# Performance work log

Measured on AMD Instinct MI355X. Metric: run time of the kernel, lower is better.

The kernel has to match this reference:

```python
import jax, jax.numpy as jnp
import numpy as np

NUM_EXPERTS = 8
IN_FEATURES = 2048
OUT_FEATURES = 2048
TOTAL_TOKENS = 32768


def setup_inputs() -> dict:
    key = jax.random.key(0)
    k1, k2, k3 = jax.random.split(key, 3)
    input_tokens = jax.random.normal(k1, (TOTAL_TOKENS, IN_FEATURES), dtype=jnp.float32)
    expert_assignments = jax.random.randint(k2, (TOTAL_TOKENS,), 0, NUM_EXPERTS, dtype=jnp.int32)
    # kaiming_uniform_ with a=sqrt(2): bound = sqrt(6 / ((1 + a^2) * fan_in)) = sqrt(2 / fan_in)
    bound = float(np.sqrt(2.0 / IN_FEATURES))
    weight = jax.random.uniform(k3, (NUM_EXPERTS, OUT_FEATURES, IN_FEATURES),
                                dtype=jnp.float32, minval=-bound, maxval=bound)
    return {"input_tokens": input_tokens, "expert_assignments": expert_assignments, "weight": weight}


def reference(input_tokens, expert_assignments, weight):
    # Grouped GEMM: out[t] = input_tokens[t] @ weight[assign[t]].T
    # Each token belongs to exactly one expert, so masked accumulation over the
    # small fixed expert set reproduces the original sort+per-expert-mm+scatter math.
    num_experts = weight.shape[0]
    out = jnp.zeros((input_tokens.shape[0], weight.shape[1]), dtype=input_tokens.dtype)
    for e in range(num_experts):
        mask = (expert_assignments == e)[:, None]  # [T, 1]
        # zero out tokens not owned by this expert before the GEMM so the
        # contribution is exact (matmul of zero rows yields zero rows)
        xe = jnp.where(mask, input_tokens, 0.0)  # [T, in]
        out = out + xe @ weight[e].T  # [T, out]
    return out
```

## Files before the change

### kernel.cpp

```cpp
#include <hip/hip_runtime.h>
#include <hip/hip_bf16.h>

#define NEXP 8
#define KIN 2048
#define NOUT 2048
#define NTOK 32768

#define BM 128
#define BN 128
#define BK 32

#define NBLK (NTOK / 256)
#define MAXTILE (NTOK / BM + NEXP - 1)

typedef unsigned int u32;
typedef unsigned short u16;
typedef __bf16 bf16x8 __attribute__((ext_vector_type(8)));
typedef float f32x4 __attribute__((ext_vector_type(4)));

__device__ __forceinline__ u16 f2bf(float f) {
    u32 u = __float_as_uint(f);
    u += 0x7FFFu + ((u >> 16) & 1u);
    return (u16)(u >> 16);
}

__device__ __forceinline__ void load_lds16(const void* g, void* l) {
    __builtin_amdgcn_global_load_lds(
        (const __attribute__((address_space(1))) u32*)g,
        (__attribute__((address_space(3))) u32*)l, 16, 0, 0);
}

__global__ void rank_k(const int* __restrict__ assign, int* __restrict__ counts,
                       int* __restrict__ rank, int* __restrict__ blockBase) {
    __shared__ int lc[NEXP];
    int t = blockIdx.x * 256 + threadIdx.x;
    if (threadIdx.x < NEXP) lc[threadIdx.x] = 0;
    __syncthreads();
    int e = assign[t];
    rank[t] = atomicAdd(&lc[e], 1);
    __syncthreads();
    if (threadIdx.x < NEXP)
        blockBase[blockIdx.x * NEXP + threadIdx.x] =
            atomicAdd(&counts[threadIdx.x], lc[threadIdx.x]);
}

__global__ void prefix_k(int* __restrict__ ctrl, int4* __restrict__ tileTable) {
    if (threadIdx.x == 0) {
        int ts = 0, tile = 0;
        for (int e = 0; e < NEXP; e++) {
            ctrl[8 + e] = ts;
            int c = ctrl[e];
            int ntile = (c + BM - 1) / BM;
            for (int i = 0; i < ntile; i++)
                tileTable[tile++] = make_int4(ts + i * BM, ts + c, e, 0);
            ts += c;
        }
        ctrl[8 + NEXP] = ts;
        for (; tile < MAXTILE; tile++) tileTable[tile] = make_int4(0, 0, 0, 0);
    }
}

__global__ void scatter_k(const int* __restrict__ assign, const int* __restrict__ ctrl,
                          const int* __restrict__ rank, const int* __restrict__ blockBase,
                          int* __restrict__ list) {
    __shared__ int base[NEXP];
    int t = blockIdx.x * 256 + threadIdx.x;
    if (threadIdx.x < NEXP)
        base[threadIdx.x] = ctrl[8 + threadIdx.x] +
                            blockBase[blockIdx.x * NEXP + threadIdx.x];
    __syncthreads();
    list[base[assign[t]] + rank[t]] = t;
}

__global__ void conv_k(const float* __restrict__ src, u16* __restrict__ dst) {
    size_t i = ((size_t)blockIdx.x * 256 + threadIdx.x) << 3;
    const float4* s = (const float4*)(src + i);
    float4 f0 = s[0], f1 = s[1];
    uint4 o;
    o.x = (u32)f2bf(f0.x) | ((u32)f2bf(f0.y) << 16);
    o.y = (u32)f2bf(f0.z) | ((u32)f2bf(f0.w) << 16);
    o.z = (u32)f2bf(f1.x) | ((u32)f2bf(f1.y) << 16);
    o.w = (u32)f2bf(f1.z) | ((u32)f2bf(f1.w) << 16);
    *(uint4*)(dst + i) = o;
}

__global__ __launch_bounds__(256, 4) void gemm_k(const u16* __restrict__ Ab,
                                                 const u16* __restrict__ Wb,
                                                 const int* __restrict__ list,
                                                 const int4* __restrict__ tileTable,
                                                 float* __restrict__ out) {
    __shared__ u16 As[BM * BK];
    __shared__ u16 Bs[BN * BK];
    __shared__ int listLds[BM];

    int4 tt = tileTable[blockIdx.y];
    int rowBase = tt.x, rowEnd = tt.y, e = tt.z;
    if (rowEnd <= rowBase) return;
    int nBase = blockIdx.x * BN;
    int tid = threadIdx.x;

    if (tid < BM) {
        int r = rowBase + tid;
        listLds[tid] = list[min(r, rowEnd - 1)];
    }
    __syncthreads();

    int sr = tid >> 2;
    int sc = tid & 3;
    int ca = (sc + (sr >> 1)) & 3;
    int tok0 = listLds[sr], tok1 = listLds[sr + 64];
    const u16* ga0 = Ab + (size_t)tok0 * KIN + ca * 8;
    const u16* ga1 = Ab + (size_t)tok1 * KIN + ca * 8;
    const u16* gb  = Wb + ((size_t)e * NOUT + nBase + sr) * KIN + ca * 8;
    char* lA = (char*)As + tid * 16;
    char* lB = (char*)Bs + tid * 16;

    int wave = tid >> 6, lane = tid & 63;
    int wm = (wave >> 1) * 64, wn = (wave & 1) * 64;
    int lm = lane & 15, kg = lane >> 4;
    int sl = (kg - (lm >> 1)) & 3;
    const u16* Ard = As + (wm + lm) * BK + sl * 8;
    const u16* Brd = Bs + (wn + lm) * BK + sl * 8;

    f32x4 acc[4][4];
#pragma unroll
    for (int i = 0; i < 4; i++)
#pragma unroll
        for (int j = 0; j < 4; j++) acc[i][j] = (f32x4){0.f, 0.f, 0.f, 0.f};

    for (int kt = 0; kt < KIN; kt += BK) {
        __syncthreads();
        load_lds16(ga0 + kt, lA);
        load_lds16(ga1 + kt, lA + 4096);
        load_lds16(gb + kt, lB);
        load_lds16(gb + (size_t)64 * KIN + kt, lB + 4096);
        __syncthreads();

        bf16x8 fa[4], fb[4];
#pragma unroll
        for (int i = 0; i < 4; i++) fa[i] = *(const bf16x8*)(Ard + i * 16 * BK);
#pragma unroll
        for (int j = 0; j < 4; j++) fb[j] = *(const bf16x8*)(Brd + j * 16 * BK);
#pragma unroll
        for (int i = 0; i < 4; i++)
#pragma unroll
            for (int j = 0; j < 4; j++)
                acc[i][j] = __builtin_amdgcn_mfma_f32_16x16x32_bf16(fa[i], fb[j], acc[i][j], 0, 0, 0);
    }

#pragma unroll
    for (int i = 0; i < 4; i++) {
        int r0 = wm + i * 16 + kg * 4;
#pragma unroll
        for (int rr = 0; rr < 4; rr++) {
            int rl = r0 + rr;
            if (rowBase + rl < rowEnd) {
                int tok = listLds[rl];
                float* orow = out + (size_t)tok * NOUT + nBase + wn + lm;
#pragma unroll
                for (int j = 0; j < 4; j++) orow[j * 16] = acc[i][j][rr];
            }
        }
    }
}

__global__ void fallback_k(const float* __restrict__ A, const int* __restrict__ assign,
                           const float* __restrict__ W, float* __restrict__ out) {
    long idx = (long)blockIdx.x * 256 + threadIdx.x;
    int t = (int)(idx >> 11);
    int n = (int)(idx & (NOUT - 1));
    int e = assign[t];
    const float4* a = (const float4*)(A + (size_t)t * KIN);
    const float4* w = (const float4*)(W + ((size_t)e * NOUT + n) * KIN);
    float s = 0.f;
    for (int k = 0; k < KIN / 4; k++) {
        float4 x = a[k], y = w[k];
        s += x.x * y.x + x.y * y.y + x.z * y.z + x.w * y.w;
    }
    out[idx] = s;
}

extern "C" void kernel_launch(void* const* d_in, const int* in_sizes, int n_in,
                              void* d_out, int out_size, void* d_ws, size_t ws_size,
                              hipStream_t stream) {
    const float* A = (const float*)d_in[0];
    const int* assign = (const int*)d_in[1];
    const float* W = (const float*)d_in[2];
    float* out = (float*)d_out;

    const size_t Ab_bytes = (size_t)NTOK * KIN * 2;
    const size_t Wb_bytes = (size_t)NEXP * NOUT * KIN * 2;
    const size_t list_bytes = (size_t)NTOK * 4;
    const size_t rank_bytes = (size_t)NTOK * 4;
    const size_t bb_bytes = (size_t)NBLK * NEXP * 4;
    const size_t ctrl_bytes = 256;
    const size_t tt_bytes = (size_t)MAXTILE * 16;
    const size_t need = Ab_bytes + Wb_bytes + list_bytes + rank_bytes +
                        bb_bytes + ctrl_bytes + tt_bytes;

    if (ws_size < need) {
        fallback_k<<<(NTOK * (long)NOUT) / 256, 256, 0, stream>>>(A, assign, W, out);
        return;
    }

    char* p = (char*)d_ws;
    u16* Ab = (u16*)p;                     p += Ab_bytes;
    u16* Wb = (u16*)p;                     p += Wb_bytes;
    int* list = (int*)p;                   p += list_bytes;
    int* rank = (int*)p;                   p += rank_bytes;
    int* blockBase = (int*)p;              p += bb_bytes;
    int* ctrl = (int*)p;                   p += ctrl_bytes;
    int4* tileTable = (int4*)p;

    hipMemsetAsync(ctrl, 0, ctrl_bytes, stream);
    rank_k<<<NBLK, 256, 0, stream>>>(assign, ctrl, rank, blockBase);
    prefix_k<<<1, 64, 0, stream>>>(ctrl, tileTable);
    scatter_k<<<NBLK, 256, 0, stream>>>(assign, ctrl, rank, blockBase, list);
    conv_k<<<(NTOK * (KIN / 8)) / 256, 256, 0, stream>>>(A, Ab);
    conv_k<<<(NEXP * NOUT * (KIN / 8)) / 256, 256, 0, stream>>>(W, Wb);
    dim3 grid(NOUT / BN, MAXTILE);
    gemm_k<<<grid, 256, 0, stream>>>(Ab, Wb, list, tileTable, out);
}
```

Baseline: 875.7 us.

## Rewrite grouped GEMM with 256x256x64 tiles and double-buffered LDS pipeline

Replaces the simple single-buffer 128x128x32 GEMM with a 512-thread 256x256x64 tile kernel. Direct-to-LDS loads are double buffered and interleaved with MFMA quads, synchronised with explicit vmcnt waits, raw barriers and setprio. LDS reads use an XOR swizzle. This targets exposed load latency and per-tile synchronisation, at the cost of 128KB of dynamic LDS, lower occupancy, and more padding waste in partial expert tiles.

```diff
diff --git a/kernel.cpp b/kernel.cpp
--- a/kernel.cpp
+++ b/kernel.cpp
@@ -6,9 +6,9 @@
 #define NOUT 2048
 #define NTOK 32768
 
-#define BM 128
-#define BN 128
-#define BK 32
+#define BM 256
+#define BN 256
+#define BK 64
 
 #define NBLK (NTOK / 256)
 #define MAXTILE (NTOK / BM + NEXP - 1)
@@ -84,84 +84,143 @@
     *(uint4*)(dst + i) = o;
 }
 
-__global__ __launch_bounds__(256, 4) void gemm_k(const u16* __restrict__ Ab,
+#define BARS() asm volatile("s_barrier" ::: "memory")
+#define WVM(N) asm volatile("s_waitcnt vmcnt(" #N ")" ::: "memory")
+
+__global__ __launch_bounds__(512, 2) void gemm_k(const u16* __restrict__ Ab,
                                                  const u16* __restrict__ Wb,
                                                  const int* __restrict__ list,
                                                  const int4* __restrict__ tileTable,
                                                  float* __restrict__ out) {
-    __shared__ u16 As[BM * BK];
-    __shared__ u16 Bs[BN * BK];
-    __shared__ int listLds[BM];
+    extern __shared__ char sh[];
+    int* listLds = (int*)(sh + 131072);
 
     int4 tt = tileTable[blockIdx.y];
     int rowBase = tt.x, rowEnd = tt.y, e = tt.z;
     if (rowEnd <= rowBase) return;
     int nBase = blockIdx.x * BN;
     int tid = threadIdx.x;
-
-    if (tid < BM) {
-        int r = rowBase + tid;
-        listLds[tid] = list[min(r, rowEnd - 1)];
-    }
-    __syncthreads();
-
-    int sr = tid >> 2;
-    int sc = tid & 3;
-    int ca = (sc + (sr >> 1)) & 3;
-    int tok0 = listLds[sr], tok1 = listLds[sr + 64];
-    const u16* ga0 = Ab + (size_t)tok0 * KIN + ca * 8;
-    const u16* ga1 = Ab + (size_t)tok1 * KIN + ca * 8;
-    const u16* gb  = Wb + ((size_t)e * NOUT + nBase + sr) * KIN + ca * 8;
-    char* lA = (char*)As + tid * 16;
-    char* lB = (char*)Bs + tid * 16;
-
-    int wave = tid >> 6, lane = tid & 63;
-    int wm = (wave >> 1) * 64, wn = (wave & 1) * 64;
-    int lm = lane & 15, kg = lane >> 4;
-    int sl = (kg - (lm >> 1)) & 3;
-    const u16* Ard = As + (wm + lm) * BK + sl * 8;
-    const u16* Brd = Bs + (wn + lm) * BK + sl * 8;
-
-    f32x4 acc[4][4];
-#pragma unroll
-    for (int i = 0; i < 4; i++)
-#pragma unroll
-        for (int j = 0; j < 4; j++) acc[i][j] = (f32x4){0.f, 0.f, 0.f, 0.f};
-
-    for (int kt = 0; kt < KIN; kt += BK) {
-        __syncthreads();
-        load_lds16(ga0 + kt, lA);
-        load_lds16(ga1 + kt, lA + 4096);
-        load_lds16(gb + kt, lB);
-        load_lds16(gb + (size_t)64 * KIN + kt, lB + 4096);
-        __syncthreads();
-
-        bf16x8 fa[4], fb[4];
-#pragma unroll
-        for (int i = 0; i < 4; i++) fa[i] = *(const bf16x8*)(Ard + i * 16 * BK);
-#pragma unroll
-        for (int j = 0; j < 4; j++) fb[j] = *(const bf16x8*)(Brd + j * 16 * BK);
-#pragma unroll
-        for (int i = 0; i < 4; i++)
-#pragma unroll
-            for (int j = 0; j < 4; j++)
-                acc[i][j] = __builtin_amdgcn_mfma_f32_16x16x32_bf16(fa[i], fb[j], acc[i][j], 0, 0, 0);
-    }
-
-#pragma unroll
-    for (int i = 0; i < 4; i++) {
-        int r0 = wm + i * 16 + kg * 4;
-#pragma unroll
-        for (int rr = 0; rr < 4; rr++) {
+    int lane = tid & 63, w = tid >> 6;
+    int wm = w >> 2, wn = w & 3;
+
+    if (tid < BM) listLds[tid] = list[min(rowBase + tid, rowEnd - 1)];
+    __syncthreads();
+
+    int srow = (w << 4) + (lane >> 3);
+    u32 ksoB = (u32)((((lane & 7) ^ (lane >> 3)) << 4));
+    u32 aO00 = (u32)listLds[srow] * 4096u + ksoB;
+    u32 aO01 = (u32)listLds[srow + 8] * 4096u + ksoB;
+    u32 aO10 = (u32)listLds[srow + 128] * 4096u + ksoB;
+    u32 aO11 = (u32)listLds[srow + 136] * 4096u + ksoB;
+    u32 bO0 = (u32)(e * NOUT + nBase + srow) * 4096u + ksoB;
+    u32 bO1 = bO0 + 128u * 4096u;
+    u32 ldsOff = (u32)((w << 11) + (lane << 4));
+
+#define STA(H, m, b) { char* d_ = sh + (b) * 65536 + (H) * 16384 + ldsOff;          \
+        load_lds16((const char*)Ab + aO##H##0 + (m) * 128, d_);                      \
+        load_lds16((const char*)Ab + aO##H##1 + (m) * 128, d_ + 1024); }
+#define STB(H, m, b) { char* d_ = sh + (b) * 65536 + 32768 + (H) * 16384 + ldsOff;   \
+        load_lds16((const char*)Wb + bO##H + (m) * 128, d_);                         \
+        load_lds16((const char*)Wb + bO##H + 32768u + (m) * 128, d_ + 1024); }
+
+    u32 s0 = (u32)((((lane >> 4) ^ (lane & 7)) << 4));
+    u32 aRow = (u32)((wm * 128 + (lane & 15)) * 128);
+    u32 bRow = (u32)(32768 + (wn * 64 + (lane & 15)) * 128);
+
+    bf16x8 ra0[4][2], ra1[4][2], rb0[2][2], rb1[2][2];
+    f32x4 acc[8][4];
+#pragma unroll
+    for (int i = 0; i < 8; ++i)
+#pragma unroll
+        for (int j = 0; j < 4; ++j) acc[i][j] = (f32x4){0.f, 0.f, 0.f, 0.f};
+
+#define RDA(dst, mf0, b) { _Pragma("unroll") for (int m_ = 0; m_ < 4; ++m_) {        \
+        const char* p_ = sh + (b) * 65536 + aRow + ((mf0) + m_) * 2048;              \
+        dst[m_][0] = *(const bf16x8*)(p_ + s0);                                      \
+        dst[m_][1] = *(const bf16x8*)(p_ + (s0 ^ 64)); } }
+#define RDB(dst, nf0, b) { _Pragma("unroll") for (int n_ = 0; n_ < 2; ++n_) {        \
+        const char* p_ = sh + (b) * 65536 + bRow + ((nf0) + n_) * 2048;              \
+        dst[n_][0] = *(const bf16x8*)(p_ + s0);                                      \
+        dst[n_][1] = *(const bf16x8*)(p_ + (s0 ^ 64)); } }
+
+#define QUAD(RA, RB, MO, NO) { __builtin_amdgcn_s_setprio(1);                        \
+    _Pragma("unroll") for (int m_ = 0; m_ < 4; ++m_)                                 \
+    _Pragma("unroll") for (int n_ = 0; n_ < 2; ++n_) {                               \
+        acc[(MO)+m_][(NO)+n_] = __builtin_amdgcn_mfma_f32_16x16x32_bf16(             \
+            RA[m_][0], RB[n_][0], acc[(MO)+m_][(NO)+n_], 0, 0, 0);                   \
+        acc[(MO)+m_][(NO)+n_] = __builtin_amdgcn_mfma_f32_16x16x32_bf16(             \
+            RA[m_][1], RB[n_][1], acc[(MO)+m_][(NO)+n_], 0, 0, 0); }                 \
+    __builtin_amdgcn_s_setprio(0); }
+
+    STA(0, 0, 0); STA(1, 0, 0); STB(0, 0, 0); STB(1, 0, 0);
+    STB(0, 1, 1); STB(1, 1, 1); STA(0, 1, 1);
+    WVM(6);
+    BARS();
+    RDA(ra0, 0, 0); RDB(rb0, 0, 0);
+
+    for (int j = 0; j < 30; ++j) {
+        int b = j & 1, nb = b ^ 1;
+        RDB(rb1, 2, b);
+        STA(1, j + 1, nb);
+        QUAD(ra0, rb0, 0, 0);
+        BARS();
+        RDA(ra1, 4, b);
+        STB(0, j + 2, b);
+        QUAD(ra0, rb1, 0, 2);
+        BARS();
+        STB(1, j + 2, b);
+        QUAD(ra1, rb0, 4, 0);
+        BARS();
+        WVM(4);
+        BARS();
+        RDA(ra0, 0, nb);
+        RDB(rb0, 0, nb);
+        STA(0, j + 2, b);
+        QUAD(ra1, rb1, 4, 2);
+        BARS();
+    }
+
+    RDB(rb1, 2, 0);
+    STA(1, 31, 1);
+    QUAD(ra0, rb0, 0, 0);
+    BARS();
+    RDA(ra1, 4, 0);
+    QUAD(ra0, rb1, 0, 2);
+    BARS();
+    QUAD(ra1, rb0, 4, 0);
+    BARS();
+    WVM(0);
+    BARS();
+    RDA(ra0, 0, 1);
+    RDB(rb0, 0, 1);
+    QUAD(ra1, rb1, 4, 2);
+    RDB(rb1, 2, 1);
+    QUAD(ra0, rb0, 0, 0);
+    RDA(ra1, 4, 1);
+    QUAD(ra0, rb1, 0, 2);
+    QUAD(ra1, rb0, 4, 0);
+    QUAD(ra1, rb1, 4, 2);
+
+    int cnt = rowEnd - rowBase;
+    int cb = nBase + wn * 64 + (lane & 15);
+#pragma unroll
+    for (int mf = 0; mf < 8; ++mf) {
+        int r0 = wm * 128 + mf * 16 + ((lane >> 4) << 2);
+#pragma unroll
+        for (int rr = 0; rr < 4; ++rr) {
             int rl = r0 + rr;
-            if (rowBase + rl < rowEnd) {
-                int tok = listLds[rl];
-                float* orow = out + (size_t)tok * NOUT + nBase + wn + lm;
-#pragma unroll
-                for (int j = 0; j < 4; j++) orow[j * 16] = acc[i][j][rr];
+            if (rl < cnt) {
+                float* orow = out + (size_t)listLds[rl] * NOUT + cb;
+#pragma unroll
+                for (int nf = 0; nf < 4; ++nf) orow[nf * 16] = acc[mf][nf][rr];
             }
         }
     }
+#undef STA
+#undef STB
+#undef RDA
+#undef RDB
+#undef QUAD
 }
 
 __global__ void fallback_k(const float* __restrict__ A, const int* __restrict__ assign,
@@ -212,6 +271,13 @@
     int* ctrl = (int*)p;                   p += ctrl_bytes;
     int4* tileTable = (int4*)p;
 
+    static bool attr_done = false;
+    if (!attr_done) {
+        hipFuncSetAttribute((const void*)gemm_k,
+                            hipFuncAttributeMaxDynamicSharedMemorySize, 132096);
+        attr_done = true;
+    }
+
     hipMemsetAsync(ctrl, 0, ctrl_bytes, stream);
     rank_k<<<NBLK, 256, 0, stream>>>(assign, ctrl, rank, blockBase);
     prefix_k<<<1, 64, 0, stream>>>(ctrl, tileTable);
@@ -219,5 +285,5 @@
     conv_k<<<(NTOK * (KIN / 8)) / 256, 256, 0, stream>>>(A, Ab);
     conv_k<<<(NEXP * NOUT * (KIN / 8)) / 256, 256, 0, stream>>>(W, Wb);
     dim3 grid(NOUT / BN, MAXTILE);
-    gemm_k<<<grid, 256, 0, stream>>>(Ab, Wb, list, tileTable, out);
-}
+    gemm_k<<<grid, 512, 132096, stream>>>(Ab, Wb, list, tileTable, out);
+}
```

After: 804.4 us. 8.1% less time.
